# Kernel optimization log

Measured on AMD Instinct MI355X. Metric: run time of the kernel, lower is better.

## Reference

```python
import jax, jax.numpy as jnp
import numpy as np

B, N = 128, 1024

def setup_inputs() -> dict:
    key = jax.random.key(0)
    k1, k2 = jax.random.split(key)
    probs = jax.random.uniform(k1, (B, N), dtype=jnp.float32)
    co_matrix = jax.random.uniform(k2, (N, N), dtype=jnp.float32)
    return {"probs": probs, "co_matrix": co_matrix}

def reference(probs, co_matrix):
    # diff[b, i, j] = probs[b, j] - probs[b, i]
    diff = probs[:, None, :] - probs[:, :, None]          # [B, N, N]
    weighted = jnp.square(diff) * co_matrix[None, :, :]   # [B, N, N]
    eps = 1e-8
    n_pos = jnp.sum((co_matrix > 0).astype(jnp.float32))
    # sum over (i, j) of mean over batch
    loss = jnp.sum(jnp.mean(weighted, axis=0)) / (n_pos + eps)
    return loss
```

## Files before the change

### kernel.cpp

```cpp
#include <hip/hip_runtime.h>


#define B_DIM 128
#define N_DIM 1024
#define TILE  64

__device__ double g_sum;
__device__ unsigned long long g_cnt;
__device__ float g_t[N_DIM];

__global__ __launch_bounds__(256) void tsq_kernel(const float* __restrict__ P) {
    int k = blockIdx.x * 256 + threadIdx.x;
    if (k == 0) g_sum = 0.0;
    if (k == 1) g_cnt = 0ull;
    float s = 0.f;
#pragma unroll 8
    for (int b = 0; b < B_DIM; ++b) {
        float v = P[b * N_DIM + k];
        s = fmaf(v, v, s);
    }
    g_t[k] = s;
}

__global__ __launch_bounds__(256) void main_kernel(const float* __restrict__ P,
                                                   const float* __restrict__ C) {
    __shared__ float Pi[B_DIM][TILE];
    __shared__ float Pj[B_DIM][TILE];
    __shared__ double wsum[4];
    __shared__ int    wcnt[4];

    const int tj_blk = blockIdx.x & 15;
    const int ti_blk = blockIdx.x >> 4;
    const int i0 = ti_blk * TILE, j0 = tj_blk * TILE;
    const int tid = threadIdx.x;

    const float4* P4 = (const float4*)P;
    float4* Pi4 = (float4*)&Pi[0][0];
    float4* Pj4 = (float4*)&Pj[0][0];
#pragma unroll
    for (int r = 0; r < 8; ++r) {
        int idx = r * 256 + tid;
        int b   = idx >> 4;
        int q   = idx & 15;
        Pi4[idx] = P4[b * (N_DIM / 4) + (i0 >> 2) + q];
        Pj4[idx] = P4[b * (N_DIM / 4) + (j0 >> 2) + q];
    }
    __syncthreads();

    const int tx = tid & 15, ty = tid >> 4;
    float g00=0,g01=0,g02=0,g03=0, g10=0,g11=0,g12=0,g13=0,
          g20=0,g21=0,g22=0,g23=0, g30=0,g31=0,g32=0,g33=0;
#pragma unroll 4
    for (int b = 0; b < B_DIM; ++b) {
        float4 a = *(const float4*)&Pi[b][ty * 4];
        float4 c = *(const float4*)&Pj[b][tx * 4];
        g00 = fmaf(a.x, c.x, g00); g01 = fmaf(a.x, c.y, g01);
        g02 = fmaf(a.x, c.z, g02); g03 = fmaf(a.x, c.w, g03);
        g10 = fmaf(a.y, c.x, g10); g11 = fmaf(a.y, c.y, g11);
        g12 = fmaf(a.y, c.z, g12); g13 = fmaf(a.y, c.w, g13);
        g20 = fmaf(a.z, c.x, g20); g21 = fmaf(a.z, c.y, g21);
        g22 = fmaf(a.z, c.z, g22); g23 = fmaf(a.z, c.w, g23);
        g30 = fmaf(a.w, c.x, g30); g31 = fmaf(a.w, c.y, g31);
        g32 = fmaf(a.w, c.z, g32); g33 = fmaf(a.w, c.w, g33);
    }
    float gm[4][4] = {{g00,g01,g02,g03},{g10,g11,g12,g13},
                      {g20,g21,g22,g23},{g30,g31,g32,g33}};

    float ti[4], tj[4];
#pragma unroll
    for (int r = 0; r < 4; ++r) ti[r] = g_t[i0 + ty * 4 + r];
#pragma unroll
    for (int c = 0; c < 4; ++c) tj[c] = g_t[j0 + tx * 4 + c];

    float acc = 0.f;
    int   cnt = 0;
    const float4* C4 = (const float4*)C;
#pragma unroll
    for (int r = 0; r < 4; ++r) {
        float4 cv = C4[(size_t)(i0 + ty * 4 + r) * (N_DIM / 4) + (j0 >> 2) + tx];
        acc = fmaf(cv.x, ti[r] + tj[0] - 2.f * gm[r][0], acc);
        acc = fmaf(cv.y, ti[r] + tj[1] - 2.f * gm[r][1], acc);
        acc = fmaf(cv.z, ti[r] + tj[2] - 2.f * gm[r][2], acc);
        acc = fmaf(cv.w, ti[r] + tj[3] - 2.f * gm[r][3], acc);
        cnt += (cv.x > 0.f) + (cv.y > 0.f) + (cv.z > 0.f) + (cv.w > 0.f);
    }

#pragma unroll
    for (int off = 32; off > 0; off >>= 1) {
        acc += __shfl_down(acc, off);
        cnt += __shfl_down(cnt, off);
    }
    const int wave = tid >> 6, lane = tid & 63;
    if (lane == 0) { wsum[wave] = (double)acc; wcnt[wave] = cnt; }
    __syncthreads();
    if (tid == 0) {
        double s = wsum[0] + wsum[1] + wsum[2] + wsum[3];
        int    c = wcnt[0] + wcnt[1] + wcnt[2] + wcnt[3];
        atomicAdd(&g_sum, s);
        atomicAdd(&g_cnt, (unsigned long long)c);
    }
}

__global__ void fin_kernel(float* __restrict__ out) {
    double npos = (double)g_cnt;
    out[0] = (float)(g_sum / ((double)B_DIM * (npos + 1e-8)));
}

extern "C" void kernel_launch(void* const* d_in, const int* in_sizes, int n_in,
                              void* d_out, int out_size, void* d_ws, size_t ws_size,
                              hipStream_t stream) {
    const float* probs = (const float*)d_in[0];
    const float* co    = (const float*)d_in[1];
    float* out = (float*)d_out;

    tsq_kernel<<<N_DIM / 256, 256, 0, stream>>>(probs);
    main_kernel<<<(N_DIM / TILE) * (N_DIM / TILE), 256, 0, stream>>>(probs, co);
    fin_kernel<<<1, 64, 0, stream>>>(out);
}
```

Baseline: 77.12 us.

## Fuse squared-norm pass into tile kernel and replace atomics with two-stage reduction

Removes the separate column squared-norm kernel: each tile block now computes the norms of its own Pi and Pj columns from the shared-memory copies it already holds. Global double atomics are replaced by per-block partial sums written to workspace, then combined by a single-block reduce kernel. Threads per block double to 512, each producing a 2x4 Gram sub-tile instead of 4x4. This cuts one kernel launch and the atomic contention, at the cost of computing the norms redundantly in every block and doing less register-level reuse per thread.

Result: faster. 65.99 us (-14.4%).

```diff
diff --git a/kernel.cpp b/kernel.cpp
--- a/kernel.cpp
+++ b/kernel.cpp
@@ -5,41 +5,27 @@
 #define N_DIM 1024
 #define TILE  64
 
-__device__ double g_sum;
-__device__ unsigned long long g_cnt;
-__device__ float g_t[N_DIM];
-
-__global__ __launch_bounds__(256) void tsq_kernel(const float* __restrict__ P) {
-    int k = blockIdx.x * 256 + threadIdx.x;
-    if (k == 0) g_sum = 0.0;
-    if (k == 1) g_cnt = 0ull;
-    float s = 0.f;
-#pragma unroll 8
-    for (int b = 0; b < B_DIM; ++b) {
-        float v = P[b * N_DIM + k];
-        s = fmaf(v, v, s);
-    }
-    g_t[k] = s;
-}
-
-__global__ __launch_bounds__(256) void main_kernel(const float* __restrict__ P,
-                                                   const float* __restrict__ C) {
+__global__ __launch_bounds__(512) void tile_kernel(const float* __restrict__ P,
+                                                   const float* __restrict__ C,
+                                                   double* __restrict__ psum,
+                                                   unsigned* __restrict__ pcnt) {
     __shared__ float Pi[B_DIM][TILE];
     __shared__ float Pj[B_DIM][TILE];
-    __shared__ double wsum[4];
-    __shared__ int    wcnt[4];
+    __shared__ float ts[2 * TILE];
+    __shared__ double wsum[8];
+    __shared__ unsigned wcnt[8];
 
+    const int tid = threadIdx.x;
     const int tj_blk = blockIdx.x & 15;
     const int ti_blk = blockIdx.x >> 4;
     const int i0 = ti_blk * TILE, j0 = tj_blk * TILE;
-    const int tid = threadIdx.x;
 
     const float4* P4 = (const float4*)P;
     float4* Pi4 = (float4*)&Pi[0][0];
     float4* Pj4 = (float4*)&Pj[0][0];
 #pragma unroll
-    for (int r = 0; r < 8; ++r) {
-        int idx = r * 256 + tid;
+    for (int r = 0; r < 4; ++r) {
+        int idx = r * 512 + tid;
         int b   = idx >> 4;
         int q   = idx & 15;
         Pi4[idx] = P4[b * (N_DIM / 4) + (i0 >> 2) + q];
@@ -47,37 +33,44 @@
     }
     __syncthreads();
 
-    const int tx = tid & 15, ty = tid >> 4;
-    float g00=0,g01=0,g02=0,g03=0, g10=0,g11=0,g12=0,g13=0,
-          g20=0,g21=0,g22=0,g23=0, g30=0,g31=0,g32=0,g33=0;
-#pragma unroll 4
+    if (tid < 2 * TILE) {
+        const float* col = (tid < TILE) ? &Pi[0][tid] : &Pj[0][tid - TILE];
+        float s = 0.f;
+#pragma unroll 8
+        for (int b = 0; b < B_DIM; ++b) {
+            float v = col[b * TILE];
+            s = fmaf(v, v, s);
+        }
+        ts[tid] = s;
+    }
+    __syncthreads();
+
+    const int tx = tid & 15;
+    const int ty = tid >> 4;
+    float g00=0,g01=0,g02=0,g03=0, g10=0,g11=0,g12=0,g13=0;
+#pragma unroll 8
     for (int b = 0; b < B_DIM; ++b) {
-        float4 a = *(const float4*)&Pi[b][ty * 4];
+        float2 a = *(const float2*)&Pi[b][ty * 2];
         float4 c = *(const float4*)&Pj[b][tx * 4];
         g00 = fmaf(a.x, c.x, g00); g01 = fmaf(a.x, c.y, g01);
         g02 = fmaf(a.x, c.z, g02); g03 = fmaf(a.x, c.w, g03);
         g10 = fmaf(a.y, c.x, g10); g11 = fmaf(a.y, c.y, g11);
         g12 = fmaf(a.y, c.z, g12); g13 = fmaf(a.y, c.w, g13);
-        g20 = fmaf(a.z, c.x, g20); g21 = fmaf(a.z, c.y, g21);
-        g22 = fmaf(a.z, c.z, g22); g23 = fmaf(a.z, c.w, g23);
-        g30 = fmaf(a.w, c.x, g30); g31 = fmaf(a.w, c.y, g31);
-        g32 = fmaf(a.w, c.z, g32); g33 = fmaf(a.w, c.w, g33);
     }
-    float gm[4][4] = {{g00,g01,g02,g03},{g10,g11,g12,g13},
-                      {g20,g21,g22,g23},{g30,g31,g32,g33}};
+    float gm[2][4] = {{g00,g01,g02,g03},{g10,g11,g12,g13}};
 
-    float ti[4], tj[4];
+    float ti[2], tj[4];
 #pragma unroll
-    for (int r = 0; r < 4; ++r) ti[r] = g_t[i0 + ty * 4 + r];
+    for (int r = 0; r < 2; ++r) ti[r] = ts[ty * 2 + r];
 #pragma unroll
-    for (int c = 0; c < 4; ++c) tj[c] = g_t[j0 + tx * 4 + c];
+    for (int c = 0; c < 4; ++c) tj[c] = ts[TILE + tx * 4 + c];
 
     float acc = 0.f;
-    int   cnt = 0;
+    unsigned cnt = 0;
     const float4* C4 = (const float4*)C;
 #pragma unroll
-    for (int r = 0; r < 4; ++r) {
-        float4 cv = C4[(size_t)(i0 + ty * 4 + r) * (N_DIM / 4) + (j0 >> 2) + tx];
+    for (int r = 0; r < 2; ++r) {
+        float4 cv = C4[(size_t)(i0 + ty * 2 + r) * (N_DIM / 4) + (j0 >> 2) + tx];
         acc = fmaf(cv.x, ti[r] + tj[0] - 2.f * gm[r][0], acc);
         acc = fmaf(cv.y, ti[r] + tj[1] - 2.f * gm[r][1], acc);
         acc = fmaf(cv.z, ti[r] + tj[2] - 2.f * gm[r][2], acc);
@@ -94,16 +87,35 @@
     if (lane == 0) { wsum[wave] = (double)acc; wcnt[wave] = cnt; }
     __syncthreads();
     if (tid == 0) {
-        double s = wsum[0] + wsum[1] + wsum[2] + wsum[3];
-        int    c = wcnt[0] + wcnt[1] + wcnt[2] + wcnt[3];
-        atomicAdd(&g_sum, s);
-        atomicAdd(&g_cnt, (unsigned long long)c);
+        double s = 0.0; unsigned c = 0;
+#pragma unroll
+        for (int w = 0; w < 8; ++w) { s += wsum[w]; c += wcnt[w]; }
+        psum[blockIdx.x] = s;
+        pcnt[blockIdx.x] = c;
     }
 }
 
-__global__ void fin_kernel(float* __restrict__ out) {
-    double npos = (double)g_cnt;
-    out[0] = (float)(g_sum / ((double)B_DIM * (npos + 1e-8)));
+__global__ __launch_bounds__(256) void reduce_kernel(const double* __restrict__ psum,
+                                                     const unsigned* __restrict__ pcnt,
+                                                     float* __restrict__ out) {
+    __shared__ double ws[4];
+    __shared__ unsigned wc[4];
+    const int tid = threadIdx.x;
+    double s = psum[tid];
+    unsigned c = pcnt[tid];
+#pragma unroll
+    for (int off = 32; off > 0; off >>= 1) {
+        s += __shfl_down(s, off);
+        c += __shfl_down(c, off);
+    }
+    const int wave = tid >> 6, lane = tid & 63;
+    if (lane == 0) { ws[wave] = s; wc[wave] = c; }
+    __syncthreads();
+    if (tid == 0) {
+        double st = ws[0] + ws[1] + ws[2] + ws[3];
+        double ct = (double)(wc[0] + wc[1] + wc[2] + wc[3]);
+        out[0] = (float)(st / ((double)B_DIM * (ct + 1e-8)));
+    }
 }
 
 extern "C" void kernel_launch(void* const* d_in, const int* in_sizes, int n_in,
@@ -113,7 +125,9 @@
     const float* co    = (const float*)d_in[1];
     float* out = (float*)d_out;
 
-    tsq_kernel<<<N_DIM / 256, 256, 0, stream>>>(probs);
-    main_kernel<<<(N_DIM / TILE) * (N_DIM / TILE), 256, 0, stream>>>(probs, co);
-    fin_kernel<<<1, 64, 0, stream>>>(out);
+    double*   psum = (double*)d_ws;
+    unsigned* pcnt = (unsigned*)((char*)d_ws + 256 * 8);
+
+    tile_kernel<<<(N_DIM / TILE) * (N_DIM / TILE), 512, 0, stream>>>(probs, co, psum, pcnt);
+    reduce_kernel<<<1, 256, 0, stream>>>(psum, pcnt, out);
 }
```
